# Kernel optimization log

Hardware: AMD Instinct MI355X
Metric: run time of the kernel (lower is better)

Reference implementation:

```python
import jax, jax.numpy as jnp
import numpy as np

BLOCK_K = 32   # BLOCK_K_SIZE_MIN in the original Triton kernel
BLOCK_N = 32   # output-block granularity of the hash


def _hash_indices(random_numbers, num_nb, num_kb, num_red_kb):
    # universal hash of (n_block, k_block) -> reduced k-block index
    r = random_numbers.astype(jnp.uint32)
    nb = jnp.arange(num_nb, dtype=jnp.uint32)[:, None]
    kb = jnp.arange(num_kb, dtype=jnp.uint32)[None, :]
    hv = (kb * r[0] + nb * r[1] + r[2]) ^ r[3]
    return (hv % jnp.uint32(num_red_kb)).astype(jnp.int32)  # [num_nb, num_kb]


def _ssl_forward(x, weight, bias, random_numbers):
    orig_shape = x.shape
    K = orig_shape[-1]
    x2 = x.reshape(-1, K)                       # [M, K]
    N, red_K = weight.shape
    num_kb = K // BLOCK_K
    num_red_kb = red_K // BLOCK_K
    num_nb = N // BLOCK_N
    h = _hash_indices(random_numbers, num_nb, num_kb, num_red_kb)  # [num_nb, num_kb]
    # Gather the virtual full weight from the reduced weight via hash indices.
    wb = weight.reshape(num_nb, BLOCK_N, num_red_kb, BLOCK_K)
    w_full = jnp.take_along_axis(wb, h[:, None, :, None], axis=2)  # [num_nb, BN, num_kb, BK]
    w_full = w_full.reshape(N, K)
    y = x2 @ w_full.T
    if bias is not None:
        y = y + bias
    return y.reshape(*orig_shape[:-1], N)


def setup_inputs() -> dict:
    key = jax.random.key(0)
    k1, k2, k3 = jax.random.split(key, 3)
    in_features, out_features, redn_factor, seed = 8192, 512, 8, 1024
    red_in = ((in_features // redn_factor + BLOCK_K - 1) // BLOCK_K) * BLOCK_K  # 1024
    x = jax.random.normal(k1, (4, 2048, in_features), dtype=jnp.float32)
    bound = 1.0 / np.sqrt(red_in)
    weight = jax.random.uniform(k2, (out_features, red_in), jnp.float32, -bound, bound)
    bias = jax.random.uniform(k3, (out_features,), jnp.float32, -bound, bound)
    rng = np.random.default_rng(seed)
    random_numbers = jnp.asarray(rng.integers(1, 2**31 - 1, size=4), dtype=jnp.int32)
    return {"x": x, "weight": weight, "bias": bias,
            "random_numbers": random_numbers, "redn_factor": redn_factor}


def reference(x, weight, bias, random_numbers, redn_factor):
    return _ssl_forward(x, weight, bias, random_numbers)
```

## Files before the change

kernel.cpp:

```cpp
#include <hip/hip_runtime.h>
#include <hip/hip_bf16.h>
#include <stdint.h>


typedef __bf16 bf16x8_t __attribute__((ext_vector_type(8)));
typedef float f32x4 __attribute__((ext_vector_type(4)));

#define BM 128
#define BN 64
#define BK 32
#define KSPLIT 2

__global__ void init_out(float* __restrict__ Out, const float* __restrict__ Bias,
                         int N, int total4) {
  int i = blockIdx.x * blockDim.x + threadIdx.x;
  if (i < total4) {
    int idx = i << 2;
    int n = idx % N;
    *(f32x4*)(Out + idx) = *(const f32x4*)(Bias + n);
  }
}

__global__ __launch_bounds__(256, 4) void ssl_gemm(
    const float* __restrict__ X,
    const float* __restrict__ W,
    const int* __restrict__ RN,
    float* __restrict__ Out,
    int M, int N, int K, int redK, uint32_t numRedKb, int mTiles, int nTiles) {
  __shared__ __align__(16) float As[2][BM * BK];

  const uint32_t r0 = (uint32_t)RN[0], r1 = (uint32_t)RN[1];
  const uint32_t r2 = (uint32_t)RN[2], r3 = (uint32_t)RN[3];
  const uint32_t redMask = numRedKb - 1u;
  const bool pow2 = (numRedKb & (numRedKb - 1u)) == 0u;

  const int id = blockIdx.x;
  const int mTile = id % mTiles;
  const int kChunk = (id / mTiles) % KSPLIT;
  const int nTile = id / (mTiles * KSPLIT);

  const int tid = threadIdx.x;
  const int wave = tid >> 6;
  const int lane = tid & 63;
  const int wm = wave >> 1, wn = wave & 1;

  const int r16 = lane & 15;
  const int x7 = lane & 7;
  const int e0 = (lane >> 4) << 3;

  const int sRow = tid >> 3;
  const int sSlot = (tid & 7) ^ (sRow & 7);
  const float* aSrc = X + (size_t)(mTile * BM + sRow) * K + sSlot * 4;

  auto stageA = [&](int buf, int kb) {
    const float* src = aSrc + (size_t)kb * BK;
#pragma unroll
    for (int p = 0; p < 4; ++p)
      __builtin_amdgcn_global_load_lds(
          (const __attribute__((address_space(1))) uint32_t*)(src + (size_t)p * 32 * K),
          (__attribute__((address_space(3))) uint32_t*)(&As[buf][p * 1024] + tid * 4),
          16, 0, 0);
  };

  const int nRow0 = nTile * BN + wn * 32;
  const uint32_t nb = (uint32_t)(nRow0 >> 5);
  const float* wRow = W + (size_t)(nRow0 + r16) * redK + e0;

  auto loadB = [&](int kb, f32x4* r) {
    const uint32_t hv = ((uint32_t)kb * r0 + nb * r1 + r2) ^ r3;
    const uint32_t h = pow2 ? (hv & redMask) : (hv % numRedKb);
#pragma unroll
    for (int ni = 0; ni < 2; ++ni) {
      const float* q = wRow + (size_t)(ni * 16) * redK + h * 32u;
      r[2 * ni]     = *(const f32x4*)(q);
      r[2 * ni + 1] = *(const f32x4*)(q + 4);
    }
  };
  auto cvtB = [&](const f32x4* s, bf16x8_t* d) {
#pragma unroll
    for (int i = 0; i < 2; ++i) {
      bf16x8_t t;
#pragma unroll
      for (int j = 0; j < 4; ++j) {
        t[j]     = (__bf16)s[2 * i][j];
        t[4 + j] = (__bf16)s[2 * i + 1][j];
      }
      d[i] = t;
    }
  };

  const int s0 = (lane >> 4) << 1;
  auto readA = [&](int buf, bf16x8_t* af) {
#pragma unroll
    for (int mi = 0; mi < 4; ++mi) {
      const int row = (wm << 6) + (mi << 4) + r16;
      const float* base = &As[buf][row * 32];
      f32x4 lo = *(const f32x4*)(base + ((s0 ^ x7) << 2));
      f32x4 hi = *(const f32x4*)(base + (((s0 + 1) ^ x7) << 2));
      bf16x8_t t;
#pragma unroll
      for (int j = 0; j < 4; ++j) {
        t[j]     = (__bf16)lo[j];
        t[4 + j] = (__bf16)hi[j];
      }
      af[mi] = t;
    }
  };

  f32x4 acc[4][2] = {};
  auto mfma8 = [&](const bf16x8_t* af, const bf16x8_t* bb) {
#pragma unroll
    for (int mi = 0; mi < 4; ++mi)
#pragma unroll
      for (int ni = 0; ni < 2; ++ni)
        acc[mi][ni] = __builtin_amdgcn_mfma_f32_16x16x32_bf16(
            af[mi], bb[ni], acc[mi][ni], 0, 0, 0);
  };

  const int numKb = K / BK;
  const int kbN = numKb / KSPLIT;
  const int kb0 = kChunk * kbN;

  f32x4 b0[4], b1[4];
  bf16x8_t af[4], bb[2];

  stageA(0, kb0);
  loadB(kb0, b0);
  if (1 < kbN) loadB(kb0 + 1, b1);
  __syncthreads();

  for (int i = 0; i < kbN; i += 2) {
    if (i + 1 < kbN) stageA(1, kb0 + i + 1);
    cvtB(b0, bb);
    if (i + 2 < kbN) loadB(kb0 + i + 2, b0);
    readA(0, af);
    mfma8(af, bb);
    __syncthreads();

    if (i + 1 < kbN) {
      if (i + 2 < kbN) stageA(0, kb0 + i + 2);
      cvtB(b1, bb);
      if (i + 3 < kbN) loadB(kb0 + i + 3, b1);
      readA(1, af);
      mfma8(af, bb);
      __syncthreads();
    }
  }

  const int mBase = mTile * BM + (wm << 6);
  const int nBase = nTile * BN + (wn << 5);
#pragma unroll
  for (int ni = 0; ni < 2; ++ni) {
    const int n = nBase + (ni << 4) + (lane & 15);
#pragma unroll
    for (int mi = 0; mi < 4; ++mi) {
      const int m0 = mBase + (mi << 4) + ((lane >> 4) << 2);
#pragma unroll
      for (int r = 0; r < 4; ++r)
        unsafeAtomicAdd(&Out[(size_t)(m0 + r) * N + n], acc[mi][ni][r]);
    }
  }
}

extern "C" void kernel_launch(void* const* d_in, const int* in_sizes, int n_in,
                              void* d_out, int out_size, void* d_ws, size_t ws_size,
                              hipStream_t stream) {
  const float* X = (const float*)d_in[0];
  const float* W = (const float*)d_in[1];
  const float* Bias = (const float*)d_in[2];
  const int* RN = (const int*)d_in[3];
  float* Out = (float*)d_out;

  const int N = in_sizes[2];
  const int M = out_size / N;
  const int K = in_sizes[0] / M;
  const int redK = in_sizes[1] / N;
  const uint32_t numRedKb = (uint32_t)(redK / 32);

  const int total4 = out_size / 4;
  init_out<<<(total4 + 255) / 256, 256, 0, stream>>>(Out, Bias, N, total4);

  const int mTiles = M / BM;
  const int nTiles = N / BN;
  dim3 grid(mTiles * KSPLIT * nTiles), block(256);
  ssl_gemm<<<grid, block, 0, stream>>>(X, W, RN, Out,
                                       M, N, K, redK, numRedKb, mTiles, nTiles);
}
```

Before: 619.2 us.

## Triple-buffer A staging with explicit waitcnt pipeline and XCD-aware block mapping

Result: no change. 612.2 us (-1.1%).

```diff
diff --git a/kernel.cpp b/kernel.cpp
--- a/kernel.cpp
+++ b/kernel.cpp
@@ -10,6 +10,7 @@
 #define BN 64
 #define BK 32
 #define KSPLIT 2
+#define NBUF 3
 
 __global__ void init_out(float* __restrict__ Out, const float* __restrict__ Bias,
                          int N, int total4) {
@@ -21,13 +22,13 @@
   }
 }
 
-__global__ __launch_bounds__(256, 4) void ssl_gemm(
+__global__ __launch_bounds__(256, 3) void ssl_gemm(
     const float* __restrict__ X,
     const float* __restrict__ W,
     const int* __restrict__ RN,
     float* __restrict__ Out,
     int M, int N, int K, int redK, uint32_t numRedKb, int mTiles, int nTiles) {
-  __shared__ __align__(16) float As[2][BM * BK];
+  __shared__ __align__(16) float As[NBUF][BM * BK];
 
   const uint32_t r0 = (uint32_t)RN[0], r1 = (uint32_t)RN[1];
   const uint32_t r2 = (uint32_t)RN[2], r3 = (uint32_t)RN[3];
@@ -35,9 +36,12 @@
   const bool pow2 = (numRedKb & (numRedKb - 1u)) == 0u;
 
   const int id = blockIdx.x;
-  const int mTile = id % mTiles;
-  const int kChunk = (id / mTiles) % KSPLIT;
-  const int nTile = id / (mTiles * KSPLIT);
+  const int xcd = id & 7;
+  const int t = id >> 3;
+  const int mTile = ((t >> 4) << 3) + xcd;
+  const int j = t & 15;
+  const int nTile = j & 7;
+  const int kChunk = j >> 3;
 
   const int tid = threadIdx.x;
   const int wave = tid >> 6;
@@ -76,39 +80,41 @@
       r[2 * ni + 1] = *(const f32x4*)(q + 4);
     }
   };
-  auto cvtB = [&](const f32x4* s, bf16x8_t* d) {
+
+  bf16x8_t af[4], bb[2];
+  auto cvtB = [&](const f32x4* s) {
 #pragma unroll
     for (int i = 0; i < 2; ++i) {
-      bf16x8_t t;
-#pragma unroll
-      for (int j = 0; j < 4; ++j) {
-        t[j]     = (__bf16)s[2 * i][j];
-        t[4 + j] = (__bf16)s[2 * i + 1][j];
+      bf16x8_t v;
+#pragma unroll
+      for (int jj = 0; jj < 4; ++jj) {
+        v[jj]     = (__bf16)s[2 * i][jj];
+        v[4 + jj] = (__bf16)s[2 * i + 1][jj];
       }
-      d[i] = t;
+      bb[i] = v;
     }
   };
 
   const int s0 = (lane >> 4) << 1;
-  auto readA = [&](int buf, bf16x8_t* af) {
+  auto readA = [&](int buf) {
 #pragma unroll
     for (int mi = 0; mi < 4; ++mi) {
       const int row = (wm << 6) + (mi << 4) + r16;
       const float* base = &As[buf][row * 32];
       f32x4 lo = *(const f32x4*)(base + ((s0 ^ x7) << 2));
       f32x4 hi = *(const f32x4*)(base + (((s0 + 1) ^ x7) << 2));
-      bf16x8_t t;
-#pragma unroll
-      for (int j = 0; j < 4; ++j) {
-        t[j]     = (__bf16)lo[j];
-        t[4 + j] = (__bf16)hi[j];
+      bf16x8_t v;
+#pragma unroll
+      for (int jj = 0; jj < 4; ++jj) {
+        v[jj]     = (__bf16)lo[jj];
+        v[4 + jj] = (__bf16)hi[jj];
       }
-      af[mi] = t;
+      af[mi] = v;
     }
   };
 
   f32x4 acc[4][2] = {};
-  auto mfma8 = [&](const bf16x8_t* af, const bf16x8_t* bb) {
+  auto mfma8 = [&]() {
 #pragma unroll
     for (int mi = 0; mi < 4; ++mi)
 #pragma unroll
@@ -121,31 +127,52 @@
   const int kbN = numKb / KSPLIT;
   const int kb0 = kChunk * kbN;
 
-  f32x4 b0[4], b1[4];
-  bf16x8_t af[4], bb[2];
-
-  stageA(0, kb0);
-  loadB(kb0, b0);
-  if (1 < kbN) loadB(kb0 + 1, b1);
-  __syncthreads();
-
-  for (int i = 0; i < kbN; i += 2) {
-    if (i + 1 < kbN) stageA(1, kb0 + i + 1);
-    cvtB(b0, bb);
-    if (i + 2 < kbN) loadB(kb0 + i + 2, b0);
-    readA(0, af);
-    mfma8(af, bb);
-    __syncthreads();
-
-    if (i + 1 < kbN) {
-      if (i + 2 < kbN) stageA(0, kb0 + i + 2);
-      cvtB(b1, bb);
-      if (i + 3 < kbN) loadB(kb0 + i + 3, b1);
-      readA(1, af);
-      mfma8(af, bb);
-      __syncthreads();
-    }
-  }
+  f32x4 bR0[4], bR1[4];
+  stageA(0, kb0 + 0); loadB(kb0 + 0, bR0);
+  stageA(1, kb0 + 1); loadB(kb0 + 1, bR1);
+
+#define KSTEP_MAIN(BI, RI, KB)                                          \
+  {                                                                     \
+    __builtin_amdgcn_sched_barrier(0);                                  \
+    asm volatile("s_waitcnt vmcnt(8)" ::: "memory");                    \
+    asm volatile("s_waitcnt lgkmcnt(0)" ::: "memory");                  \
+    __builtin_amdgcn_s_barrier();                                       \
+    __builtin_amdgcn_sched_barrier(0);                                  \
+    stageA((BI + 2) % NBUF, (KB) + 2);                                  \
+    cvtB(bR##RI);                                                       \
+    loadB((KB) + 2, bR##RI);                                            \
+    __builtin_amdgcn_sched_barrier(0);                                  \
+    readA(BI);                                                          \
+    mfma8();                                                            \
+  }
+
+  for (int i = 0; i < kbN - 2; i += 6) {
+    KSTEP_MAIN(0, 0, kb0 + i);
+    KSTEP_MAIN(1, 1, kb0 + i + 1);
+    KSTEP_MAIN(2, 0, kb0 + i + 2);
+    KSTEP_MAIN(0, 1, kb0 + i + 3);
+    KSTEP_MAIN(1, 0, kb0 + i + 4);
+    KSTEP_MAIN(2, 1, kb0 + i + 5);
+  }
+#undef KSTEP_MAIN
+
+  __builtin_amdgcn_sched_barrier(0);
+  asm volatile("s_waitcnt vmcnt(8)" ::: "memory");
+  asm volatile("s_waitcnt lgkmcnt(0)" ::: "memory");
+  __builtin_amdgcn_s_barrier();
+  __builtin_amdgcn_sched_barrier(0);
+  cvtB(bR0);
+  readA(0);
+  mfma8();
+
+  __builtin_amdgcn_sched_barrier(0);
+  asm volatile("s_waitcnt vmcnt(0)" ::: "memory");
+  asm volatile("s_waitcnt lgkmcnt(0)" ::: "memory");
+  __builtin_amdgcn_s_barrier();
+  __builtin_amdgcn_sched_barrier(0);
+  cvtB(bR1);
+  readA(1);
+  mfma8();
 
   const int mBase = mTile * BM + (wm << 6);
   const int nBase = nTile * BN + (wn << 5);
@@ -182,7 +209,7 @@
 
   const int mTiles = M / BM;
   const int nTiles = N / BN;
-  dim3 grid(mTiles * KSPLIT * nTiles), block(256);
+  dim3 grid(mTiles * nTiles * KSPLIT), block(256);
   ssl_gemm<<<grid, block, 0, stream>>>(X, W, RN, Out,
                                        M, N, K, redK, numRedKb, mTiles, nTiles);
 }
```
